# Performance work log

Hardware: AMD Instinct MI355X
Metric: run time of the kernel (lower is better)

The kernel has to match this reference:

```python
import jax, jax.numpy as jnp
import numpy as np

N_NODES = 100000
N_EDGES = 1600000
N_GRAPHS = 128
H = 64          # hidden_channels_gin
L = 3           # num_layers
IN_X = 4
IN_E = 8
G_DIM = H * L   # pooled concat dim = hidden_channels_global
OUT = 1


def _w(k, shape):
    return (jax.random.normal(k, shape, jnp.float32) * 0.1)


def setup_inputs() -> dict:
    key = jax.random.key(0)
    ks = jax.random.split(key, 24)
    inp = {
        'x': jax.random.normal(ks[0], (N_NODES, IN_X), jnp.float32),
        'edge_index': jax.random.randint(ks[1], (2, N_EDGES), 0, N_NODES),
        'batch': jnp.sort(jax.random.randint(ks[2], (N_NODES,), 0, N_GRAPHS)),
        'edge_attr': jax.random.normal(ks[3], (N_EDGES, IN_E), jnp.float32),
        # node embedding MLP (MLPembd: Linear-ReLU-Linear-ReLU-Linear)
        'nW1': _w(ks[4], (IN_X, H)), 'nb1': jnp.zeros((H,), jnp.float32),
        'nW2': _w(ks[5], (H, H)),    'nb2': jnp.zeros((H,), jnp.float32),
        'nW3': _w(ks[6], (H, H)),    'nb3': jnp.zeros((H,), jnp.float32),
        # edge embedding MLP (gin_MLP_layers[0])
        'eW1': _w(ks[7], (IN_E, H)), 'eb1': jnp.zeros((H,), jnp.float32),
        'eW2': _w(ks[8], (H, H)),    'eb2': jnp.zeros((H,), jnp.float32),
        'eW3': _w(ks[9], (H, H)),    'eb3': jnp.zeros((H,), jnp.float32),
        # GINE layers: trainable eps + 2-layer MLP nn per layer (stacked over L)
        'gine_eps': jnp.zeros((L,), jnp.float32),
        'gW1': _w(ks[10], (L, H, H)), 'gb1': jnp.zeros((L, H), jnp.float32),
        'gW2': _w(ks[11], (L, H, H)), 'gb2': jnp.zeros((L, H), jnp.float32),
        # output MLP: Linear - BN(eval) - LeakyReLU - (Dropout eval) - Linear
        'oW1': _w(ks[12], (G_DIM, G_DIM)), 'ob1': jnp.zeros((G_DIM,), jnp.float32),
        'ogamma': jnp.ones((G_DIM,), jnp.float32), 'obeta': jnp.zeros((G_DIM,), jnp.float32),
        'oW2': _w(ks[13], (G_DIM, OUT)), 'ob2': jnp.zeros((OUT,), jnp.float32),
    }
    return inp


def _mlp3(x, W1, b1, W2, b2, W3, b3):
    x = jax.nn.relu(x @ W1 + b1)
    x = jax.nn.relu(x @ W2 + b2)
    return x @ W3 + b3


def _forward(x, edge_index, batch, edge_attr,
             nW1, nb1, nW2, nb2, nW3, nb3,
             eW1, eb1, eW2, eb2, eW3, eb3,
             gine_eps, gW1, gb1, gW2, gb2,
             oW1, ob1, ogamma, obeta, oW2, ob2):
    src, dst = edge_index[0], edge_index[1]
    h = _mlp3(x, nW1, nb1, nW2, nb2, nW3, nb3)                    # [N, H]
    ea = _mlp3(edge_attr, eW1, eb1, eW2, eb2, eW3, eb3)           # [E, H]
    pooled = []
    for l in range(L):  # fixed small layer count
        msg = jax.nn.leaky_relu(h[src] + ea)                      # [E, H] gather + add
        agg = jax.ops.segment_max(msg, dst, num_segments=N_NODES) # max aggregation
        agg = jnp.where(jnp.isfinite(agg), agg, 0.0)              # isolated nodes -> 0
        z = (1.0 + gine_eps[l]) * h + agg
        h = jax.nn.leaky_relu(z @ gW1[l] + gb1[l]) @ gW2[l] + gb2[l]
        pooled.append(jax.ops.segment_max(h, batch, num_segments=N_GRAPHS))
    hp = jnp.concatenate(pooled, axis=1)                          # [G, H*L]
    y = hp @ oW1 + ob1
    y = ogamma * y + obeta            # eval-mode BatchNorm1d (running mean=0, var=1)
    y = jax.nn.leaky_relu(y)          # Dropout inactive at inference
    logits = y @ oW2 + ob2            # [G, 1]
    return logits, jax.nn.sigmoid(logits)


def reference(x, edge_index, batch, edge_attr,
              nW1, nb1, nW2, nb2, nW3, nb3,
              eW1, eb1, eW2, eb2, eW3, eb3,
              gine_eps, gW1, gb1, gW2, gb2,
              oW1, ob1, ogamma, obeta, oW2, ob2):
    return _forward(x, edge_index, batch, edge_attr,
                    nW1, nb1, nW2, nb2, nW3, nb3,
                    eW1, eb1, eW2, eb2, eW3, eb3,
                    gine_eps, gW1, gb1, gW2, gb2,
                    oW1, ob1, ogamma, obeta, oW2, ob2)
```

## Files before the change

kernel.cpp:

```cpp
#include <hip/hip_runtime.h>
#include <hip/hip_bf16.h>

#define LRELU(x) ((x) > 0.0f ? (x) : 0.01f * (x))

typedef __attribute__((ext_vector_type(4))) short bf16x4;
typedef __attribute__((ext_vector_type(4))) float f32x4;

__device__ __forceinline__ unsigned fenc(float f) {
    unsigned u = __float_as_uint(f);
    return (u & 0x80000000u) ? ~u : (u | 0x80000000u);
}
__device__ __forceinline__ float fdec(unsigned u) {
    return (u & 0x80000000u) ? __uint_as_float(u & 0x7fffffffu) : __uint_as_float(~u);
}
__device__ __forceinline__ short f2bf(float f) {
    __hip_bfloat16 b = __float2bfloat16(f);
    return *reinterpret_cast<short*>(&b);
}
__device__ __forceinline__ float bf2f(short s) {
    return __uint_as_float(((unsigned)(unsigned short)s) << 16);
}

__device__ __forceinline__ f32x4 mfma16(bf16x4 a, bf16x4 b, f32x4 c) {
#if __has_builtin(__builtin_amdgcn_mfma_f32_16x16x16bf16_1k)
    return __builtin_amdgcn_mfma_f32_16x16x16bf16_1k(a, b, c, 0, 0, 0);
#else
    asm("v_mfma_f32_16x16x16_bf16 %0, %1, %2, %0" : "+v"(c) : "v"(a), "v"(b));
    return c;
#endif
}

__global__ __launch_bounds__(256) void hist_kernel(const int* __restrict__ ei,
                                                   int* __restrict__ deg, int E)
{
    const int stride = gridDim.x * blockDim.x;
    for (int e = blockIdx.x * blockDim.x + threadIdx.x; e < E; e += stride)
        atomicAdd(&deg[ei[E + e]], 1);
}

__global__ __launch_bounds__(1024) void scan_kernel(const int* __restrict__ deg,
                                                    int* __restrict__ rowptr,
                                                    int* __restrict__ cursor, int N)
{
    __shared__ int wsum[16];
    __shared__ int tiletot;
    const int lane = threadIdx.x & 63;
    const int w    = threadIdx.x >> 6;
    int carry = 0;
    for (int base = 0; base < N; base += 4096) {
        const int i = base + (int)threadIdx.x * 4;
        int4 v = {0, 0, 0, 0};
        if (i + 3 < N) {
            v = *reinterpret_cast<const int4*>(deg + i);
        } else {
            if (i < N)     v.x = deg[i];
            if (i + 1 < N) v.y = deg[i + 1];
            if (i + 2 < N) v.z = deg[i + 2];
        }
        const int tot = v.x + v.y + v.z + v.w;
        int s = tot;
#pragma unroll
        for (int off = 1; off < 64; off <<= 1) {
            int t = __shfl_up(s, off);
            if (lane >= off) s += t;
        }
        if (lane == 63) wsum[w] = s;
        __syncthreads();
        if (threadIdx.x == 0) {
            int acc = 0;
#pragma unroll
            for (int k = 0; k < 16; ++k) { int t = wsum[k]; wsum[k] = acc; acc += t; }
            tiletot = acc;
        }
        __syncthreads();
        const int excl = carry + wsum[w] + (s - tot);
        int4 o;
        o.x = excl; o.y = excl + v.x; o.z = o.y + v.y; o.w = o.z + v.z;
        if (i + 3 < N) {
            *reinterpret_cast<int4*>(rowptr + i) = o;
            *reinterpret_cast<int4*>(cursor + i) = o;
        } else {
            if (i < N)     { rowptr[i] = o.x;     cursor[i] = o.x; }
            if (i + 1 < N) { rowptr[i + 1] = o.y; cursor[i + 1] = o.y; }
            if (i + 2 < N) { rowptr[i + 2] = o.z; cursor[i + 2] = o.z; }
        }
        carry += tiletot;
        __syncthreads();
    }
    if (threadIdx.x == 0) rowptr[N] = carry;
}

__global__ __launch_bounds__(256) void scatter_kernel(
    const int* __restrict__ ei, int* __restrict__ cursor,
    int2* __restrict__ pack, int E)
{
    const int stride = gridDim.x * blockDim.x;
    for (int e = blockIdx.x * blockDim.x + threadIdx.x; e < E; e += stride) {
        const int d = ei[E + e];
        const int p = atomicAdd(&cursor[d], 1);
        pack[p] = make_int2(ei[e], e);
    }
}

__global__ __launch_bounds__(256) void edge_mlp_mfma(
    const float* __restrict__ eattr, const int2* __restrict__ pack,
    const float* __restrict__ W1, const float* __restrict__ b1,
    const float* __restrict__ W2, const float* __restrict__ b2,
    const float* __restrict__ W3, const float* __restrict__ b3,
    short* __restrict__ eout, int E)
{
    const int lane = threadIdx.x & 63;
    const int el   = lane & 15;
    const int g    = lane >> 4;

    bf16x4 w1f[4];
    bf16x4 w2f[4][4];
    bf16x4 w3f[4][4];
    f32x4  bf1[4], bf2[4], bf3[4];
#pragma unroll
    for (int t = 0; t < 4; ++t) {
        const int c = t * 16 + el;
#pragma unroll
        for (int j = 0; j < 4; ++j) {
            const int k = g * 4 + j;
            w1f[t][j] = (k < 8) ? f2bf(W1[k * 64 + c]) : (short)0;
        }
#pragma unroll
        for (int kb = 0; kb < 4; ++kb) {
#pragma unroll
            for (int j = 0; j < 4; ++j) {
                const int k = kb * 16 + g * 4 + j;
                w2f[t][kb][j] = f2bf(W2[k * 64 + c]);
                w3f[t][kb][j] = f2bf(W3[k * 64 + c]);
            }
        }
        const float4 v1 = *reinterpret_cast<const float4*>(b1 + t * 16 + g * 4);
        const float4 v2 = *reinterpret_cast<const float4*>(b2 + t * 16 + g * 4);
        const float4 v3 = *reinterpret_cast<const float4*>(b3 + t * 16 + g * 4);
        bf1[t][0] = v1.x; bf1[t][1] = v1.y; bf1[t][2] = v1.z; bf1[t][3] = v1.w;
        bf2[t][0] = v2.x; bf2[t][1] = v2.y; bf2[t][2] = v2.z; bf2[t][3] = v2.w;
        bf3[t][0] = v3.x; bf3[t][1] = v3.y; bf3[t][2] = v3.z; bf3[t][3] = v3.w;
    }

    const int nblk = (E + 15) >> 4;
    const int wid  = (int)((blockIdx.x * blockDim.x + threadIdx.x) >> 6);
    const int nw   = (int)((gridDim.x * blockDim.x) >> 6);

    for (int eb = wid; eb < nblk; eb += nw) {
        const int e  = eb * 16 + el;
        const int ec = min(e, E - 1);
        const int eid = pack[ec].y;

        bf16x4 bfr = (bf16x4)0;
        if (g < 2) {
            const float4 av = *reinterpret_cast<const float4*>(eattr + (size_t)eid * 8 + g * 4);
            bfr[0] = f2bf(av.x); bfr[1] = f2bf(av.y);
            bfr[2] = f2bf(av.z); bfr[3] = f2bf(av.w);
        }

        f32x4  acc[4];
        bf16x4 act[4];

#pragma unroll
        for (int t = 0; t < 4; ++t) acc[t] = mfma16(w1f[t], bfr, bf1[t]);
#pragma unroll
        for (int t = 0; t < 4; ++t)
#pragma unroll
            for (int j = 0; j < 4; ++j) act[t][j] = f2bf(fmaxf(acc[t][j], 0.0f));

#pragma unroll
        for (int t = 0; t < 4; ++t) {
            f32x4 a = bf2[t];
#pragma unroll
            for (int kb = 0; kb < 4; ++kb) a = mfma16(w2f[t][kb], act[kb], a);
            acc[t] = a;
        }
#pragma unroll
        for (int t = 0; t < 4; ++t)
#pragma unroll
            for (int j = 0; j < 4; ++j) act[t][j] = f2bf(fmaxf(acc[t][j], 0.0f));

#pragma unroll
        for (int t = 0; t < 4; ++t) {
            f32x4 a = bf3[t];
#pragma unroll
            for (int kb = 0; kb < 4; ++kb) a = mfma16(w3f[t][kb], act[kb], a);
            bf16x4 o;
#pragma unroll
            for (int j = 0; j < 4; ++j) o[j] = f2bf(a[j]);
            if (e < E)
                *reinterpret_cast<bf16x4*>(eout + (size_t)e * 64 + t * 16 + g * 4) = o;
        }
    }
}

__global__ __launch_bounds__(256) void node_mlp_mfma(
    const float* __restrict__ x,
    const float* __restrict__ W1, const float* __restrict__ b1,
    const float* __restrict__ W2, const float* __restrict__ b2,
    const float* __restrict__ W3, const float* __restrict__ b3,
    short* __restrict__ hout, int N)
{
    const int lane = threadIdx.x & 63;
    const int el   = lane & 15;
    const int g    = lane >> 6 == 0 ? (lane >> 4) : 0;

    bf16x4 w1f[4];
    bf16x4 w2f[4][4];
    bf16x4 w3f[4][4];
    f32x4  bf1[4], bf2[4], bf3[4];
#pragma unroll
    for (int t = 0; t < 4; ++t) {
        const int c = t * 16 + el;
#pragma unroll
        for (int j = 0; j < 4; ++j) {
            const int k = g * 4 + j;
            w1f[t][j] = (k < 4) ? f2bf(W1[k * 64 + c]) : (short)0;
        }
#pragma unroll
        for (int kb = 0; kb < 4; ++kb) {
#pragma unroll
            for (int j = 0; j < 4; ++j) {
                const int k = kb * 16 + g * 4 + j;
                w2f[t][kb][j] = f2bf(W2[k * 64 + c]);
                w3f[t][kb][j] = f2bf(W3[k * 64 + c]);
            }
        }
        const float4 v1 = *reinterpret_cast<const float4*>(b1 + t * 16 + g * 4);
        const float4 v2 = *reinterpret_cast<const float4*>(b2 + t * 16 + g * 4);
        const float4 v3 = *reinterpret_cast<const float4*>(b3 + t * 16 + g * 4);
        bf1[t][0] = v1.x; bf1[t][1] = v1.y; bf1[t][2] = v1.z; bf1[t][3] = v1.w;
        bf2[t][0] = v2.x; bf2[t][1] = v2.y; bf2[t][2] = v2.z; bf2[t][3] = v2.w;
        bf3[t][0] = v3.x; bf3[t][1] = v3.y; bf3[t][2] = v3.z; bf3[t][3] = v3.w;
    }

    const int nblk = (N + 15) >> 4;
    const int wid  = (int)((blockIdx.x * blockDim.x + threadIdx.x) >> 6);
    const int nw   = (int)((gridDim.x * blockDim.x) >> 6);

    for (int nb = wid; nb < nblk; nb += nw) {
        const int n  = nb * 16 + el;
        const int nc = min(n, N - 1);

        bf16x4 bfr = (bf16x4)0;
        if (g == 0) {
            const float4 xv = *reinterpret_cast<const float4*>(x + (size_t)nc * 4);
            bfr[0] = f2bf(xv.x); bfr[1] = f2bf(xv.y);
            bfr[2] = f2bf(xv.z); bfr[3] = f2bf(xv.w);
        }

        f32x4  acc[4];
        bf16x4 act[4];
#pragma unroll
        for (int t = 0; t < 4; ++t) acc[t] = mfma16(w1f[t], bfr, bf1[t]);
#pragma unroll
        for (int t = 0; t < 4; ++t)
#pragma unroll
            for (int j = 0; j < 4; ++j) act[t][j] = f2bf(fmaxf(acc[t][j], 0.0f));

#pragma unroll
        for (int t = 0; t < 4; ++t) {
            f32x4 a = bf2[t];
#pragma unroll
            for (int kb = 0; kb < 4; ++kb) a = mfma16(w2f[t][kb], act[kb], a);
            acc[t] = a;
        }
#pragma unroll
        for (int t = 0; t < 4; ++t)
#pragma unroll
            for (int j = 0; j < 4; ++j) act[t][j] = f2bf(fmaxf(acc[t][j], 0.0f));

#pragma unroll
        for (int t = 0; t < 4; ++t) {
            f32x4 a = bf3[t];
#pragma unroll
            for (int kb = 0; kb < 4; ++kb) a = mfma16(w3f[t][kb], act[kb], a);
            bf16x4 o;
#pragma unroll
            for (int j = 0; j < 4; ++j) o[j] = f2bf(a[j]);
            if (n < N)
                *reinterpret_cast<bf16x4*>(hout + (size_t)n * 64 + t * 16 + g * 4) = o;
        }
    }
}

__global__ __launch_bounds__(256) void agg_kernel(
    const short* __restrict__ h_in, short* __restrict__ z_out,
    const int* __restrict__ rowptr, const int2* __restrict__ pack,
    const short* __restrict__ ea,
    const float* __restrict__ geps, int l, int N)
{
    const int lane = threadIdx.x & 63;
    const int g    = lane >> 4;
    const int el   = lane & 15;
    const float ope = 1.0f + geps[l];

    const int nwave = gridDim.x * 4;
    const int w     = blockIdx.x * 4 + (threadIdx.x >> 6);
    const int chunk = (N + nwave - 1) / nwave;
    const int n0 = w * chunk;
    const int n1 = min(N, n0 + chunk);
    if (n0 >= n1) return;

    int r0 = rowptr[n0];
    for (int n = n0; n < n1; ++n) {
        const int r1 = rowptr[n + 1];

        float m0 = -INFINITY, m1 = -INFINITY, m2 = -INFINITY, m3 = -INFINITY;
        for (int r = r0; r < r1; r += 16) {
#pragma unroll
            for (int u = 0; u < 4; ++u) {
                const int rc = min(r + u * 4 + g, r1 - 1);
                const int s  = pack[rc].x;
                const bf16x4 hv = *reinterpret_cast<const bf16x4*>(h_in + (size_t)s * 64 + el * 4);
                const bf16x4 ev = *reinterpret_cast<const bf16x4*>(ea + (size_t)rc * 64 + el * 4);
                float c0 = bf2f(hv[0]) + bf2f(ev[0]);
                float c1 = bf2f(hv[1]) + bf2f(ev[1]);
                float c2 = bf2f(hv[2]) + bf2f(ev[2]);
                float c3 = bf2f(hv[3]) + bf2f(ev[3]);
                c0 = LRELU(c0); c1 = LRELU(c1); c2 = LRELU(c2); c3 = LRELU(c3);
                m0 = fmaxf(m0, c0); m1 = fmaxf(m1, c1);
                m2 = fmaxf(m2, c2); m3 = fmaxf(m3, c3);
            }
        }
        m0 = fmaxf(m0, __shfl_xor(m0, 16)); m0 = fmaxf(m0, __shfl_xor(m0, 32));
        m1 = fmaxf(m1, __shfl_xor(m1, 16)); m1 = fmaxf(m1, __shfl_xor(m1, 32));
        m2 = fmaxf(m2, __shfl_xor(m2, 16)); m2 = fmaxf(m2, __shfl_xor(m2, 32));
        m3 = fmaxf(m3, __shfl_xor(m3, 16)); m3 = fmaxf(m3, __shfl_xor(m3, 32));

        if (g == 0) {
            const bf16x4 hn = *reinterpret_cast<const bf16x4*>(h_in + (size_t)n * 64 + el * 4);
            bf16x4 zo;
            zo[0] = f2bf(ope * bf2f(hn[0]) + ((m0 == -INFINITY) ? 0.0f : m0));
            zo[1] = f2bf(ope * bf2f(hn[1]) + ((m1 == -INFINITY) ? 0.0f : m1));
            zo[2] = f2bf(ope * bf2f(hn[2]) + ((m2 == -INFINITY) ? 0.0f : m2));
            zo[3] = f2bf(ope * bf2f(hn[3]) + ((m3 == -INFINITY) ? 0.0f : m3));
            *reinterpret_cast<bf16x4*>(z_out + (size_t)n * 64 + el * 4) = zo;
        }
        r0 = r1;
    }
}

__global__ __launch_bounds__(256) void mlp_pool_kernel(
    const short* __restrict__ z, short* __restrict__ h_out,
    const int* __restrict__ batch,
    const float* __restrict__ gW1, const float* __restrict__ gb1,
    const float* __restrict__ gW2, const float* __restrict__ gb2,
    unsigned* __restrict__ pooled, int l, int N)
{
    const int lane = threadIdx.x & 63;
    const int el   = lane & 15;
    const int g    = lane >> 4;

    const float* W1 = gW1 + (size_t)l * 4096;
    const float* W2 = gW2 + (size_t)l * 4096;
    bf16x4 w1f[4][4], w2f[4][4];
    f32x4  bA[4], bB[4];
#pragma unroll
    for (int t = 0; t < 4; ++t) {
        const int c = t * 16 + el;
#pragma unroll
        for (int kb = 0; kb < 4; ++kb) {
#pragma unroll
            for (int j = 0; j < 4; ++j) {
                const int k = kb * 16 + g * 4 + j;
                w1f[t][kb][j] = f2bf(W1[k * 64 + c]);
                w2f[t][kb][j] = f2bf(W2[k * 64 + c]);
            }
        }
        const float4 v1 = *reinterpret_cast<const float4*>(gb1 + l * 64 + t * 16 + g * 4);
        const float4 v2 = *reinterpret_cast<const float4*>(gb2 + l * 64 + t * 16 + g * 4);
        bA[t][0] = v1.x; bA[t][1] = v1.y; bA[t][2] = v1.z; bA[t][3] = v1.w;
        bB[t][0] = v2.x; bB[t][1] = v2.y; bB[t][2] = v2.z; bB[t][3] = v2.w;
    }

    const int nblk = (N + 15) >> 4;
    const int wid  = (int)((blockIdx.x * blockDim.x + threadIdx.x) >> 6);
    const int nw   = (int)((gridDim.x * blockDim.x) >> 6);

    for (int nb = wid; nb < nblk; nb += nw) {
        const int n  = nb * 16 + el;
        const bool valid = (n < N);
        const int nc = valid ? n : (N - 1);

        bf16x4 zf[4];
#pragma unroll
        for (int kb = 0; kb < 4; ++kb)
            zf[kb] = *reinterpret_cast<const bf16x4*>(z + (size_t)nc * 64 + kb * 16 + g * 4);

        f32x4  acc[4];
        bf16x4 act[4];
#pragma unroll
        for (int t = 0; t < 4; ++t) {
            f32x4 a = bA[t];
#pragma unroll
            for (int kb = 0; kb < 4; ++kb) a = mfma16(w1f[t][kb], zf[kb], a);
            acc[t] = a;
        }
#pragma unroll
        for (int t = 0; t < 4; ++t)
#pragma unroll
            for (int j = 0; j < 4; ++j) act[t][j] = f2bf(LRELU(acc[t][j]));

#pragma unroll
        for (int t = 0; t < 4; ++t) {
            f32x4 a = bB[t];
#pragma unroll
            for (int kb = 0; kb < 4; ++kb) a = mfma16(w2f[t][kb], act[kb], a);
            acc[t] = a;
        }

#pragma unroll
        for (int t = 0; t < 4; ++t) {
            bf16x4 o;
#pragma unroll
            for (int j = 0; j < 4; ++j) o[j] = f2bf(acc[t][j]);
            if (valid)
                *reinterpret_cast<bf16x4*>(h_out + (size_t)n * 64 + t * 16 + g * 4) = o;
        }

        const int gbl = batch[nc];
        const int gb_first = __shfl(gbl, 0);
        const int gb_last  = __shfl(gbl, 15);
        if (gb_first == gb_last) {
#pragma unroll
            for (int t = 0; t < 4; ++t) {
#pragma unroll
                for (int j = 0; j < 4; ++j) {
                    float v = valid ? acc[t][j] : -INFINITY;
                    v = fmaxf(v, __shfl_xor(v, 1));
                    v = fmaxf(v, __shfl_xor(v, 2));
                    v = fmaxf(v, __shfl_xor(v, 4));
                    v = fmaxf(v, __shfl_xor(v, 8));
                    if (el == 0)
                        atomicMax(&pooled[gb_first * 192 + l * 64 + t * 16 + g * 4 + j], fenc(v));
                }
            }
        } else if (valid) {
#pragma unroll
            for (int t = 0; t < 4; ++t)
#pragma unroll
                for (int j = 0; j < 4; ++j)
                    atomicMax(&pooled[gbl * 192 + l * 64 + t * 16 + g * 4 + j], fenc(acc[t][j]));
        }
    }
}

__global__ __launch_bounds__(192) void out_kernel(
    const unsigned* __restrict__ pooled,
    const float* __restrict__ oW1, const float* __restrict__ ob1,
    const float* __restrict__ ogamma, const float* __restrict__ obeta,
    const float* __restrict__ oW2, const float* __restrict__ ob2,
    float* __restrict__ out)
{
    __shared__ float hp[192];
    __shared__ float partial[3];
    const int c = threadIdx.x;
    const int g = blockIdx.x;

    const unsigned u = pooled[g * 192 + c];
    hp[c] = (u == 0u) ? -INFINITY : fdec(u);
    __syncthreads();

    float y = ob1[c];
#pragma unroll 4
    for (int k = 0; k < 192; ++k)
        y += hp[k] * oW1[k * 192 + c];
    y = ogamma[c] * y + obeta[c];
    y = LRELU(y);
    float contrib = y * oW2[c];

#pragma unroll
    for (int off = 32; off > 0; off >>= 1)
        contrib += __shfl_xor(contrib, off);
    if ((threadIdx.x & 63) == 0) partial[threadIdx.x >> 6] = contrib;
    __syncthreads();
    if (threadIdx.x == 0) {
        const float logit = partial[0] + partial[1] + partial[2] + ob2[0];
        out[g] = logit;
        out[128 + g] = 1.0f / (1.0f + expf(-logit));
    }
}

extern "C" void kernel_launch(void* const* d_in, const int* in_sizes, int n_in,
                              void* d_out, int out_size, void* d_ws, size_t ws_size,
                              hipStream_t stream)
{
    const float* x     = (const float*)d_in[0];
    const int*   ei    = (const int*)d_in[1];
    const int*   batch = (const int*)d_in[2];
    const float* eattr = (const float*)d_in[3];
    const float* nW1 = (const float*)d_in[4],  *nb1 = (const float*)d_in[5];
    const float* nW2 = (const float*)d_in[6],  *nb2 = (const float*)d_in[7];
    const float* nW3 = (const float*)d_in[8],  *nb3 = (const float*)d_in[9];
    const float* eW1 = (const float*)d_in[10], *eb1 = (const float*)d_in[11];
    const float* eW2 = (const float*)d_in[12], *eb2 = (const float*)d_in[13];
    const float* eW3 = (const float*)d_in[14], *eb3 = (const float*)d_in[15];
    const float* geps = (const float*)d_in[16];
    const float* gW1 = (const float*)d_in[17], *gb1 = (const float*)d_in[18];
    const float* gW2 = (const float*)d_in[19], *gb2 = (const float*)d_in[20];
    const float* oW1 = (const float*)d_in[21], *ob1 = (const float*)d_in[22];
    const float* ogamma = (const float*)d_in[23], *obeta = (const float*)d_in[24];
    const float* oW2 = (const float*)d_in[25], *ob2 = (const float*)d_in[26];
    float* out = (float*)d_out;

    const int N = in_sizes[0] / 4;
    const int E = in_sizes[3] / 8;
    const size_t EP = ((size_t)E + 15) & ~(size_t)15;

    char* ws = (char*)d_ws;
    size_t off = 0;
    auto take = [&](size_t bytes) { char* p = ws + off; off += (bytes + 255) & ~(size_t)255; return p; };
    short*    ea     = (short*)take(EP * 64 * sizeof(short));
    short*    h0     = (short*)take((size_t)N * 64 * sizeof(short));
    short*    h1     = (short*)take((size_t)N * 64 * sizeof(short));
    int2*     pack   = (int2*)take((size_t)E * sizeof(int2));
    short*    zbuf   = (short*)take((size_t)N * 64 * sizeof(short));
    int*      rowptr = (int*)take(((size_t)N + 1) * sizeof(int));
    unsigned* pooled = (unsigned*)take(128 * 192 * sizeof(unsigned));
    int* deg    = (int*)h1;
    int* cursor = (int*)((char*)h1 + (((size_t)N * sizeof(int) + 255) & ~(size_t)255));
    (void)ws_size;

    hipMemsetAsync(pooled, 0, 128 * 192 * sizeof(unsigned), stream);
    hipMemsetAsync(deg, 0, (size_t)N * sizeof(int), stream);

    hist_kernel<<<2048, 256, 0, stream>>>(ei, deg, E);
    scan_kernel<<<1, 1024, 0, stream>>>(deg, rowptr, cursor, N);
    node_mlp_mfma<<<1024, 256, 0, stream>>>(x, nW1, nb1, nW2, nb2, nW3, nb3, h0, N);
    scatter_kernel<<<2048, 256, 0, stream>>>(ei, cursor, pack, E);
    edge_mlp_mfma<<<2048, 256, 0, stream>>>(eattr, pack, eW1, eb1, eW2, eb2, eW3, eb3, ea, E);

    for (int l = 0; l < 3; ++l) {
        const short* hi = (l & 1) ? h1 : h0;
        short*       ho = (l & 1) ? h0 : h1;
        agg_kernel<<<2048, 256, 0, stream>>>(hi, zbuf, rowptr, pack, ea, geps, l, N);
        mlp_pool_kernel<<<1024, 256, 0, stream>>>(zbuf, ho, batch,
                                                  gW1, gb1, gW2, gb2, pooled, l, N);
    }

    out_kernel<<<128, 192, 0, stream>>>(pooled, oW1, ob1, ogamma, obeta, oW2, ob2, out);
}
```

Baseline: 774.3 us.

## Record per-edge rank during histogram to make CSR scatter atomic-free

The histogram kernel now stores the atomicAdd return value as each edge's rank within its destination. The scatter kernel then computes pack positions as rowptr[dst]+rank without a second atomic pass, and the cursor array is no longer needed. Degree counters are padded to 16-byte stride to spread atomic contention, and both edge kernels process four edges per thread with int4 loads. The cost is an extra E-sized rank buffer written and read, a larger degree memset, and strided scan reads. Edge order within a node may differ from before, which is harmless for max aggregation.

```diff
diff --git a/kernel.cpp b/kernel.cpp
--- a/kernel.cpp
+++ b/kernel.cpp
@@ -31,16 +31,31 @@
 }
 
 __global__ __launch_bounds__(256) void hist_kernel(const int* __restrict__ ei,
-                                                   int* __restrict__ deg, int E)
-{
-    const int stride = gridDim.x * blockDim.x;
-    for (int e = blockIdx.x * blockDim.x + threadIdx.x; e < E; e += stride)
-        atomicAdd(&deg[ei[E + e]], 1);
-}
-
-__global__ __launch_bounds__(1024) void scan_kernel(const int* __restrict__ deg,
-                                                    int* __restrict__ rowptr,
-                                                    int* __restrict__ cursor, int N)
+                                                   int* __restrict__ deg_p,
+                                                   int* __restrict__ rank, int E)
+{
+    const int stride = gridDim.x * blockDim.x * 4;
+    const bool vec = ((E & 3) == 0);
+    for (int e4 = (blockIdx.x * blockDim.x + threadIdx.x) * 4; e4 < E; e4 += stride) {
+        if (vec && e4 + 3 < E) {
+            const int4 d = *reinterpret_cast<const int4*>(ei + E + e4);
+            int4 r;
+            r.x = atomicAdd(&deg_p[(size_t)d.x * 4], 1);
+            r.y = atomicAdd(&deg_p[(size_t)d.y * 4], 1);
+            r.z = atomicAdd(&deg_p[(size_t)d.z * 4], 1);
+            r.w = atomicAdd(&deg_p[(size_t)d.w * 4], 1);
+            *reinterpret_cast<int4*>(rank + e4) = r;
+        } else {
+            for (int k = 0; k < 4 && e4 + k < E; ++k) {
+                const int d = ei[E + e4 + k];
+                rank[e4 + k] = atomicAdd(&deg_p[(size_t)d * 4], 1);
+            }
+        }
+    }
+}
+
+__global__ __launch_bounds__(1024) void scan_kernel(const int* __restrict__ deg_p,
+                                                    int* __restrict__ rowptr, int N)
 {
     __shared__ int wsum[16];
     __shared__ int tiletot;
@@ -50,13 +65,10 @@
     for (int base = 0; base < N; base += 4096) {
         const int i = base + (int)threadIdx.x * 4;
         int4 v = {0, 0, 0, 0};
-        if (i + 3 < N) {
-            v = *reinterpret_cast<const int4*>(deg + i);
-        } else {
-            if (i < N)     v.x = deg[i];
-            if (i + 1 < N) v.y = deg[i + 1];
-            if (i + 2 < N) v.z = deg[i + 2];
-        }
+        if (i < N)     v.x = deg_p[(size_t)i * 4];
+        if (i + 1 < N) v.y = deg_p[(size_t)(i + 1) * 4];
+        if (i + 2 < N) v.z = deg_p[(size_t)(i + 2) * 4];
+        if (i + 3 < N) v.w = deg_p[(size_t)(i + 3) * 4];
         const int tot = v.x + v.y + v.z + v.w;
         int s = tot;
 #pragma unroll
@@ -78,11 +90,10 @@
         o.x = excl; o.y = excl + v.x; o.z = o.y + v.y; o.w = o.z + v.z;
         if (i + 3 < N) {
             *reinterpret_cast<int4*>(rowptr + i) = o;
-            *reinterpret_cast<int4*>(cursor + i) = o;
         } else {
-            if (i < N)     { rowptr[i] = o.x;     cursor[i] = o.x; }
-            if (i + 1 < N) { rowptr[i + 1] = o.y; cursor[i + 1] = o.y; }
-            if (i + 2 < N) { rowptr[i + 2] = o.z; cursor[i + 2] = o.z; }
+            if (i < N)     rowptr[i] = o.x;
+            if (i + 1 < N) rowptr[i + 1] = o.y;
+            if (i + 2 < N) rowptr[i + 2] = o.z;
         }
         carry += tiletot;
         __syncthreads();
@@ -91,14 +102,26 @@
 }
 
 __global__ __launch_bounds__(256) void scatter_kernel(
-    const int* __restrict__ ei, int* __restrict__ cursor,
-    int2* __restrict__ pack, int E)
-{
-    const int stride = gridDim.x * blockDim.x;
-    for (int e = blockIdx.x * blockDim.x + threadIdx.x; e < E; e += stride) {
-        const int d = ei[E + e];
-        const int p = atomicAdd(&cursor[d], 1);
-        pack[p] = make_int2(ei[e], e);
+    const int* __restrict__ ei, const int* __restrict__ rank,
+    const int* __restrict__ rowptr, int2* __restrict__ pack, int E)
+{
+    const int stride = gridDim.x * blockDim.x * 4;
+    const bool vec = ((E & 3) == 0);
+    for (int e4 = (blockIdx.x * blockDim.x + threadIdx.x) * 4; e4 < E; e4 += stride) {
+        if (vec && e4 + 3 < E) {
+            const int4 s  = *reinterpret_cast<const int4*>(ei + e4);
+            const int4 d  = *reinterpret_cast<const int4*>(ei + E + e4);
+            const int4 rk = *reinterpret_cast<const int4*>(rank + e4);
+            pack[rowptr[d.x] + rk.x] = make_int2(s.x, e4 + 0);
+            pack[rowptr[d.y] + rk.y] = make_int2(s.y, e4 + 1);
+            pack[rowptr[d.z] + rk.z] = make_int2(s.z, e4 + 2);
+            pack[rowptr[d.w] + rk.w] = make_int2(s.w, e4 + 3);
+        } else {
+            for (int k = 0; k < 4 && e4 + k < E; ++k) {
+                const int e = e4 + k;
+                pack[rowptr[ei[E + e]] + rank[e]] = make_int2(ei[e], e);
+            }
+        }
     }
 }
 
@@ -203,7 +226,7 @@
 {
     const int lane = threadIdx.x & 63;
     const int el   = lane & 15;
-    const int g    = lane >> 6 == 0 ? (lane >> 4) : 0;
+    const int g    = lane >> 4;
 
     bf16x4 w1f[4];
     bf16x4 w2f[4][4];
@@ -516,19 +539,20 @@
     short*    h1     = (short*)take((size_t)N * 64 * sizeof(short));
     int2*     pack   = (int2*)take((size_t)E * sizeof(int2));
     short*    zbuf   = (short*)take((size_t)N * 64 * sizeof(short));
+    int*      rank   = (int*)take((size_t)E * sizeof(int));
     int*      rowptr = (int*)take(((size_t)N + 1) * sizeof(int));
     unsigned* pooled = (unsigned*)take(128 * 192 * sizeof(unsigned));
-    int* deg    = (int*)h1;
-    int* cursor = (int*)((char*)h1 + (((size_t)N * sizeof(int) + 255) & ~(size_t)255));
+    int* deg_p = (int*)h1;
     (void)ws_size;
 
     hipMemsetAsync(pooled, 0, 128 * 192 * sizeof(unsigned), stream);
-    hipMemsetAsync(deg, 0, (size_t)N * sizeof(int), stream);
-
-    hist_kernel<<<2048, 256, 0, stream>>>(ei, deg, E);
-    scan_kernel<<<1, 1024, 0, stream>>>(deg, rowptr, cursor, N);
+    hipMemsetAsync(deg_p, 0, (size_t)N * 4 * sizeof(int), stream);
+
+    const int gEdge = (E / 4 + 255) / 256 + 1;
+    hist_kernel<<<gEdge, 256, 0, stream>>>(ei, deg_p, rank, E);
+    scan_kernel<<<1, 1024, 0, stream>>>(deg_p, rowptr, N);
     node_mlp_mfma<<<1024, 256, 0, stream>>>(x, nW1, nb1, nW2, nb2, nW3, nb3, h0, N);
-    scatter_kernel<<<2048, 256, 0, stream>>>(ei, cursor, pack, E);
+    scatter_kernel<<<gEdge, 256, 0, stream>>>(ei, rank, rowptr, pack, E);
     edge_mlp_mfma<<<2048, 256, 0, stream>>>(eattr, pack, eW1, eb1, eW2, eb2, eW3, eb3, ea, E);
 
     for (int l = 0; l < 3; ++l) {
```

New measurement: 713.9 us (median of 4 runs). -7.8%, faster.
